# Kernel tuning notes

Hardware: AMD Instinct MI355X
Metric: run time of the kernel (lower is better)

## Reference

```python
import jax, jax.numpy as jnp
import numpy as np

H = 16       # num_heads
D = 128      # head_dim
SCALE = 1.0 / np.sqrt(D).astype(np.float32)


def setup_inputs() -> dict:
    key = jax.random.key(0)
    ks = jax.random.split(key, 5)
    B, S, C = 2, 2048, 2048
    x = jax.random.normal(ks[0], (B, S, C), dtype=jnp.float32)
    # nn.Linear stores weight as [out_features, in_features]; scale ~ kaiming-ish
    s = 1.0 / np.sqrt(C)
    wq = jax.random.normal(ks[1], (C, C), dtype=jnp.float32) * s
    wk = jax.random.normal(ks[2], (C, C), dtype=jnp.float32) * s
    wv = jax.random.normal(ks[3], (C, C), dtype=jnp.float32) * s
    wo = jax.random.normal(ks[4], (C, C), dtype=jnp.float32) * s
    return {"x": x, "wq": wq, "wk": wk, "wv": wv, "wo": wo}


def reference(x, wq, wk, wv, wo):
    B, S, C = x.shape
    # projections: nn.Linear(x) = x @ W.T
    q = (x @ wq.T).reshape(B, S, H, D).transpose(0, 2, 1, 3)  # [B,H,S,D]
    k = (x @ wk.T).reshape(B, S, H, D).transpose(0, 2, 1, 3)
    v = (x @ wv.T).reshape(B, S, H, D).transpose(0, 2, 1, 3)
    scores = jnp.einsum('bhqd,bhkd->bhqk', q, k) * SCALE      # [B,H,S,S]
    attn = jax.nn.softmax(scores, axis=-1)
    out = jnp.einsum('bhqk,bhkd->bhqd', attn, v)              # [B,H,S,D]
    out = out.transpose(0, 2, 1, 3).reshape(B, S, H * D)
    return out @ wo.T
```

## Files before the change

kernel.cpp:

```cpp
#include <hip/hip_runtime.h>
#include <hip/hip_bf16.h>
#include <cstdint>
#include <cstddef>

typedef __bf16 bf16_t;
typedef __bf16 bf8_t __attribute__((ext_vector_type(8)));
typedef float f4_t __attribute__((ext_vector_type(4)));
typedef float f8_t __attribute__((ext_vector_type(8)));

#define DEV static __device__ __forceinline__

DEV f4_t mfma16(bf8_t a, bf8_t b, f4_t c) {
    return __builtin_amdgcn_mfma_f32_16x16x32_bf16(a, b, c, 0, 0, 0);
}

DEV bf8_t cvt8(f8_t v) {
    bf8_t r;
#pragma unroll
    for (int i = 0; i < 8; ++i) r[i] = (bf16_t)v[i];
    return r;
}

DEV void load_lds16(const bf16_t* g, bf16_t* l) {
    __builtin_amdgcn_global_load_lds(
        (const __attribute__((address_space(1))) uint32_t*)g,
        (__attribute__((address_space(3))) uint32_t*)l,
        16, 0, 0);
}

__global__ __launch_bounds__(256) void cvt_fused(const float* __restrict__ x,
                                                 const float* __restrict__ wq,
                                                 const float* __restrict__ wk,
                                                 const float* __restrict__ wv,
                                                 bf16_t* __restrict__ xb,
                                                 bf16_t* __restrict__ wqkvb) {
    const int bid = blockIdx.x;
    const float* src;
    bf16_t* dst;
    int base;
    if (bid < 4096) {
        src = x; dst = xb; base = bid;
    } else {
        const int seg = (bid - 4096) >> 11;
        src = (seg == 0) ? wq : (seg == 1) ? wk : wv;
        dst = wqkvb + (size_t)seg * 4194304;
        base = (bid - 4096) & 2047;
    }
    const size_t i = ((size_t)base * 256 + threadIdx.x) * 8;
    const f8_t v = *(const f8_t*)&src[i];
    *(bf8_t*)&dst[i] = cvt8(v);
}

__global__ __launch_bounds__(256) void cvt_bf16(const float* __restrict__ in,
                                                bf16_t* __restrict__ out, int n8) {
    const int i = blockIdx.x * 256 + threadIdx.x;
    if (i < n8) {
        const f8_t v = *(const f8_t*)&in[(size_t)i * 8];
        *(bf8_t*)&out[(size_t)i * 8] = cvt8(v);
    }
}

DEV void stage_half(const bf16_t* X, int row0, int rb, int kt, bf16_t* bufX,
                    int wave, int srow, int scol) {
#pragma unroll
    for (int kk = 0; kk < 2; ++kk)
        load_lds16(X + (size_t)(row0 + rb + wave * 16 + srow) * 2048 + kt * 64 + kk * 32 + scol,
                   bufX + kk * 8192 + (rb + wave * 16) * 32);
}

__global__ __launch_bounds__(512, 2) void gemm256(const bf16_t* __restrict__ A,
                                                  const bf16_t* __restrict__ B,
                                                  bf16_t* __restrict__ Cq,
                                                  bf16_t* __restrict__ Ck,
                                                  bf16_t* __restrict__ Cv) {
    __shared__ bf16_t smem[65536];

    const int tid = threadIdx.x, lane = tid & 63, wave = tid >> 6;
    const int wr = wave >> 2, wc = wave & 3;
    const int q4 = lane >> 4, r16 = lane & 15;
    const int srow = lane >> 2;
    const int scol = ((lane & 3) ^ ((lane >> 3) & 3)) * 8;
    const int rkey = (r16 >> 1) & 3;

    int wg = blockIdx.y * 24 + blockIdx.x;
    wg = (wg & 7) * 48 + (wg >> 3);
    const int bm0 = (wg / 24) * 256;
    const int bn0 = (wg % 24) * 256;

    f4_t acc[8][4] = {};

    {
        bf16_t* b0 = smem;
        bf16_t* b1 = smem + 32768;
        stage_half(A, bm0, 0,   0, b0,          wave, srow, scol);
        stage_half(A, bm0, 128, 0, b0,          wave, srow, scol);
        stage_half(B, bn0, 0,   0, b0 + 16384,  wave, srow, scol);
        stage_half(B, bn0, 128, 0, b0 + 16384,  wave, srow, scol);
        stage_half(B, bn0, 0,   1, b1 + 16384,  wave, srow, scol);
        stage_half(B, bn0, 128, 1, b1 + 16384,  wave, srow, scol);
        asm volatile("s_waitcnt vmcnt(4)" ::: "memory");
        __builtin_amdgcn_s_barrier();
    }

    for (int t = 0; t < 32; ++t) {
        bf16_t* buf  = smem + (t & 1) * 32768;
        bf16_t* bufN = smem + ((t + 1) & 1) * 32768;

        bf8_t bq[4][2];
#pragma unroll
        for (int p = 0; p < 4; ++p) {
            if (p == 0) {
#pragma unroll
                for (int n = 0; n < 4; ++n)
#pragma unroll
                    for (int kk = 0; kk < 2; ++kk)
                        bq[n][kk] = *(const bf8_t*)&buf[16384 + kk * 8192 +
                                                       (wc * 64 + n * 16 + r16) * 32 +
                                                       (q4 ^ rkey) * 8];
            }
            bf8_t af[2][2];
#pragma unroll
            for (int i = 0; i < 2; ++i)
#pragma unroll
                for (int kk = 0; kk < 2; ++kk)
                    af[i][kk] = *(const bf8_t*)&buf[kk * 8192 +
                                                    (wr * 128 + (2 * p + i) * 16 + r16) * 32 +
                                                    (q4 ^ rkey) * 8];

            if (p == 0 && t + 1 < 32) {
                stage_half(A, bm0, 0,   t + 1, bufN, wave, srow, scol);
                stage_half(A, bm0, 128, t + 1, bufN, wave, srow, scol);
            }
            if (p == 1 && t + 2 < 32)
                stage_half(B, bn0, 0,   t + 2, buf + 16384, wave, srow, scol);
            if (p == 2 && t + 2 < 32)
                stage_half(B, bn0, 128, t + 2, buf + 16384, wave, srow, scol);

            __builtin_amdgcn_s_barrier();
            asm volatile("s_waitcnt lgkmcnt(0)" ::: "memory");
            __builtin_amdgcn_s_setprio(1);
#pragma unroll
            for (int kk = 0; kk < 2; ++kk)
#pragma unroll
                for (int i = 0; i < 2; ++i)
#pragma unroll
                    for (int n = 0; n < 4; ++n)
                        acc[2 * p + i][n] = mfma16(af[i][kk], bq[n][kk], acc[2 * p + i][n]);
            __builtin_amdgcn_s_setprio(0);
            if (p == 3) {
                if (t < 30) {
                    asm volatile("s_waitcnt vmcnt(4)" ::: "memory");
                } else {
                    asm volatile("s_waitcnt vmcnt(0)" ::: "memory");
                }
            }
            __builtin_amdgcn_s_barrier();
        }
    }

    __syncthreads();

    bf16_t* strip = smem + wave * 4608;
    if (bn0 < 4096) {
        bf16_t* dst = (bn0 < 2048) ? Cq : Ck;
        const int nb = (bn0 & 2047) + wc * 64;
#pragma unroll
        for (int P = 0; P < 2; ++P) {
#pragma unroll
            for (int i = 0; i < 4; ++i)
#pragma unroll
                for (int n = 0; n < 4; ++n)
#pragma unroll
                    for (int r = 0; r < 4; ++r)
                        strip[(i * 16 + q4 * 4 + r) * 72 + n * 16 + r16] =
                            (bf16_t)acc[P * 4 + i][n][r];
            asm volatile("s_waitcnt lgkmcnt(0)" ::: "memory");
#pragma unroll
            for (int it = 0; it < 8; ++it) {
                const int row = it * 8 + (lane >> 3);
                const int c = (lane & 7) * 8;
                *(bf8_t*)&dst[(size_t)(bm0 + wr * 128 + P * 64 + row) * 2048 + nb + c] =
                    *(const bf8_t*)&strip[row * 72 + c];
            }
            asm volatile("s_waitcnt lgkmcnt(0)" ::: "memory");
        }
    } else {
        const int bb = bm0 >> 11;
        const int s0 = bm0 & 2047;
#pragma unroll
        for (int P = 0; P < 2; ++P) {
#pragma unroll
            for (int i = 0; i < 4; ++i)
#pragma unroll
                for (int n = 0; n < 4; ++n)
#pragma unroll
                    for (int r = 0; r < 4; ++r)
                        strip[(n * 16 + r16) * 72 + i * 16 + q4 * 4 + r] =
                            (bf16_t)acc[P * 4 + i][n][r];
            asm volatile("s_waitcnt lgkmcnt(0)" ::: "memory");
#pragma unroll
            for (int it = 0; it < 8; ++it) {
                const int nrow = it * 8 + (lane >> 3);
                const int c = (lane & 7) * 8;
                const int dg = (bn0 - 4096) + wc * 64 + nrow;
                const int h = dg >> 7, d = dg & 127;
                *(bf8_t*)&Cv[(((size_t)(bb * 16 + h) * 128 + d) << 11) + s0 + wr * 128 + P * 64 + c] =
                    *(const bf8_t*)&strip[nrow * 72 + c];
            }
            asm volatile("s_waitcnt lgkmcnt(0)" ::: "memory");
        }
    }
}

template <int MODE>
__global__ __launch_bounds__(256) void gemm_m97(const bf16_t* __restrict__ A,
                                                const bf16_t* __restrict__ B,
                                                void* __restrict__ C0,
                                                bf16_t* __restrict__ C1,
                                                bf16_t* __restrict__ C2,
                                                int N, int K) {
    constexpr int SMEMN = (MODE == 0) ? 128 * 136 : 8192;
    __shared__ bf16_t smem[SMEMN];
    bf16_t* As = smem;
    bf16_t* Bs = smem + 4096;

    const int tid = threadIdx.x;
    const int lane = tid & 63;
    const int wave = tid >> 6;
    const int bm0 = blockIdx.y * 128;
    const int bn0 = blockIdx.x * 128;
    const int wm = (wave >> 1) * 64;
    const int wn = (wave & 1) * 64;
    const int q4 = lane >> 4;
    const int r16 = lane & 15;

    const int srow = lane >> 2;
    const int scol = (((lane & 3) ^ ((lane >> 3) & 3))) * 8;
    const int rkey = (r16 >> 1) & 3;

    f4_t acc[4][4] = {};

    for (int k0 = 0; k0 < K; k0 += 32) {
        __syncthreads();
        load_lds16(A + (size_t)(bm0 + wave * 16 + srow) * K + k0 + scol, As + wave * 16 * 32);
        load_lds16(A + (size_t)(bm0 + 64 + wave * 16 + srow) * K + k0 + scol,
                   As + (64 + wave * 16) * 32);
        load_lds16(B + (size_t)(bn0 + wave * 16 + srow) * K + k0 + scol, Bs + wave * 16 * 32);
        load_lds16(B + (size_t)(bn0 + 64 + wave * 16 + srow) * K + k0 + scol,
                   Bs + (64 + wave * 16) * 32);
        __syncthreads();

        bf8_t af[4], bfr[4];
#pragma unroll
        for (int i = 0; i < 4; ++i)
            af[i] = *(const bf8_t*)&As[(wm + i * 16 + r16) * 32 + (q4 ^ rkey) * 8];
#pragma unroll
        for (int j = 0; j < 4; ++j)
            bfr[j] = *(const bf8_t*)&Bs[(wn + j * 16 + r16) * 32 + (q4 ^ rkey) * 8];
#pragma unroll
        for (int i = 0; i < 4; ++i)
#pragma unroll
            for (int j = 0; j < 4; ++j)
                acc[i][j] = mfma16(af[i], bfr[j], acc[i][j]);
    }

    if (MODE == 1) {
        float* C = (float*)C0;
#pragma unroll
        for (int i = 0; i < 4; ++i)
#pragma unroll
            for (int j = 0; j < 4; ++j)
#pragma unroll
                for (int r = 0; r < 4; ++r) {
                    const int m = bm0 + wm + i * 16 + q4 * 4 + r;
                    const int n = bn0 + wn + j * 16 + r16;
                    C[(size_t)m * 2048 + n] = acc[i][j][r];
                }
        return;
    }

    __syncthreads();
    if (bn0 < 4096) {
        bf16_t* dst = (bn0 < 2048) ? (bf16_t*)C0 : C1;
        const int nbase = bn0 & 2047;
#pragma unroll
        for (int i = 0; i < 4; ++i)
#pragma unroll
            for (int j = 0; j < 4; ++j)
#pragma unroll
                for (int r = 0; r < 4; ++r)
                    smem[(wm + i * 16 + q4 * 4 + r) * 136 + wn + j * 16 + r16] =
                        (bf16_t)acc[i][j][r];
        __syncthreads();
#pragma unroll
        for (int it = 0; it < 8; ++it) {
            const int idx = it * 256 + tid;
            const int m = idx >> 4;
            const int nc = (idx & 15) * 8;
            *(bf8_t*)&dst[(size_t)(bm0 + m) * 2048 + nbase + nc] =
                *(const bf8_t*)&smem[m * 136 + nc];
        }
    } else {
#pragma unroll
        for (int i = 0; i < 4; ++i)
#pragma unroll
            for (int j = 0; j < 4; ++j)
#pragma unroll
                for (int r = 0; r < 4; ++r)
                    smem[(wn + j * 16 + r16) * 136 + wm + i * 16 + q4 * 4 + r] =
                        (bf16_t)acc[i][j][r];
        __syncthreads();
        const int bb = bm0 >> 11;
        const int s0 = bm0 & 2047;
        const int nh0 = bn0 - 4096;
#pragma unroll
        for (int it = 0; it < 8; ++it) {
            const int idx = it * 256 + tid;
            const int n = idx >> 4;
            const int mc = (idx & 15) * 8;
            const bf8_t v = *(const bf8_t*)&smem[n * 136 + mc];
            const int dg = nh0 + n;
            const int h = dg >> 7, d = dg & 127;
            *(bf8_t*)&C2[(((size_t)(bb * 16 + h) * 128 + d) << 11) + s0 + mc] = v;
        }
    }
}

__global__ __launch_bounds__(256) void flash5(const bf16_t* __restrict__ Q,
                                              const bf16_t* __restrict__ K,
                                              const bf16_t* __restrict__ VT,
                                              bf16_t* __restrict__ O) {
    constexpr int S = 2048, C = 2048;
    constexpr float SCL = 0.08838834764831845f * 1.4426950408889634f;
    __shared__ bf16_t Ks[4 * 64 * 32];
    __shared__ bf16_t Vs[2 * 128 * 32];
    __shared__ bf16_t Ps[4][32 * 72];

    const int tid = threadIdx.x, lane = tid & 63, wave = tid >> 6;
    const int q4 = lane >> 4, r16 = lane & 15;
    const int bh = blockIdx.y, b = bh >> 4, h = bh & 15;
    const int q0 = blockIdx.x * 128 + wave * 32;

    const size_t qrow = (size_t)b * S + q0;
    const bf16_t* Qp0 = Q + (qrow + r16) * C + h * 128;
    const bf16_t* Qp1 = Q + (qrow + 16 + r16) * C + h * 128;
    const bf16_t* Kbase = K + (size_t)b * S * C + h * 128;
    const bf16_t* Vbase = VT + (size_t)bh * 128 * S;
    bf16_t* Pw = &Ps[wave][0];

    const int srow = lane >> 2;
    const int scol = (((lane & 3) ^ ((lane >> 3) & 3))) * 8;
    const int rkey = (r16 >> 1) & 3;

    bf8_t aq0[4], aq1[4];
#pragma unroll
    for (int kk = 0; kk < 4; ++kk) {
        aq0[kk] = *(const bf8_t*)&Qp0[kk * 32 + q4 * 8];
        aq1[kk] = *(const bf8_t*)&Qp1[kk * 32 + q4 * 8];
    }

    bf8_t ones;
#pragma unroll
    for (int i = 0; i < 8; ++i) ones[i] = (bf16_t)1.0f;

    f4_t o0[8] = {}, o1[8] = {};
    f4_t lacc0 = {}, lacc1 = {};

    for (int kv0 = 0; kv0 < S; kv0 += 64) {
        __syncthreads();
#pragma unroll
        for (int r0 = 0; r0 < 64; r0 += 16)
            load_lds16(Kbase + (size_t)(kv0 + r0 + srow) * C + wave * 32 + scol,
                       Ks + wave * 2048 + r0 * 32);
        {
            const int kkp = wave >> 1;
            const int rb = (wave & 1) * 64;
#pragma unroll
            for (int r0 = 0; r0 < 64; r0 += 16)
                load_lds16(Vbase + (size_t)(rb + r0 + srow) * S + kv0 + kkp * 32 + scol,
                           Vs + kkp * 4096 + (rb + r0) * 32);
        }
        __syncthreads();

        f4_t s4a[4] = {}, s4b[4] = {};
#pragma unroll
        for (int kk = 0; kk < 4; ++kk) {
#pragma unroll
            for (int j = 0; j < 4; ++j) {
                const bf8_t bk =
                    *(const bf8_t*)&Ks[kk * 2048 + (j * 16 + r16) * 32 + (q4 ^ rkey) * 8];
                s4a[j] = mfma16(aq0[kk], bk, s4a[j]);
                s4b[j] = mfma16(aq1[kk], bk, s4b[j]);
            }
        }

#pragma unroll
        for (int r = 0; r < 4; ++r)
#pragma unroll
            for (int j = 0; j < 4; ++j) {
                Pw[(q4 * 4 + r) * 72 + j * 16 + r16] = (bf16_t)exp2f(s4a[j][r] * SCL);
                Pw[(16 + q4 * 4 + r) * 72 + j * 16 + r16] = (bf16_t)exp2f(s4b[j][r] * SCL);
            }
        asm volatile("s_waitcnt lgkmcnt(0)" ::: "memory");

        bf8_t ap0[2], ap1[2];
#pragma unroll
        for (int kkp = 0; kkp < 2; ++kkp) {
            ap0[kkp] = *(const bf8_t*)&Pw[r16 * 72 + kkp * 32 + q4 * 8];
            ap1[kkp] = *(const bf8_t*)&Pw[(16 + r16) * 72 + kkp * 32 + q4 * 8];
        }

#pragma unroll
        for (int kkp = 0; kkp < 2; ++kkp) {
            lacc0 = mfma16(ap0[kkp], ones, lacc0);
            lacc1 = mfma16(ap1[kkp], ones, lacc1);
        }

#pragma unroll
        for (int t = 0; t < 8; ++t) {
#pragma unroll
            for (int kkp = 0; kkp < 2; ++kkp) {
                const bf8_t bv =
                    *(const bf8_t*)&Vs[kkp * 4096 + (t * 16 + r16) * 32 + (q4 ^ rkey) * 8];
                o0[t] = mfma16(ap0[kkp], bv, o0[t]);
                o1[t] = mfma16(ap1[kkp], bv, o1[t]);
            }
        }
    }

    f4_t inv0, inv1;
#pragma unroll
    for (int r = 0; r < 4; ++r) {
        inv0[r] = 1.0f / lacc0[r];
        inv1[r] = 1.0f / lacc1[r];
    }
#pragma unroll
    for (int t = 0; t < 8; ++t)
#pragma unroll
        for (int r = 0; r < 4; ++r) {
            O[(qrow + q4 * 4 + r) * C + h * 128 + t * 16 + r16] = (bf16_t)(o0[t][r] * inv0[r]);
            O[(qrow + 16 + q4 * 4 + r) * C + h * 128 + t * 16 + r16] =
                (bf16_t)(o1[t][r] * inv1[r]);
        }
}

extern "C" void kernel_launch(void* const* d_in, const int* in_sizes, int n_in,
                              void* d_out, int out_size, void* d_ws, size_t ws_size,
                              hipStream_t stream) {
    const float* x  = (const float*)d_in[0];
    const float* wq = (const float*)d_in[1];
    const float* wk = (const float*)d_in[2];
    const float* wv = (const float*)d_in[3];
    const float* wo = (const float*)d_in[4];

    bf16_t* ws = (bf16_t*)d_ws;
    bf16_t* xb   = ws;
    bf16_t* Wqkv = ws + 8388608;
    bf16_t* Qb   = ws + 20971520;
    bf16_t* Kb   = ws + 29360128;
    bf16_t* Vt   = ws + 37748736;
    bf16_t* Wob  = xb;
    bf16_t* At   = Wqkv;

    cvt_fused<<<10240, 256, 0, stream>>>(x, wq, wk, wv, xb, Wqkv);

    gemm256<<<dim3(24, 16), 512, 0, stream>>>(xb, Wqkv, Qb, Kb, Vt);

    cvt_bf16<<<2048, 256, 0, stream>>>(wo, Wob, 524288);

    flash5<<<dim3(16, 32), 256, 0, stream>>>(Qb, Kb, Vt, At);

    gemm_m97<1><<<dim3(16, 32), 256, 0, stream>>>(At, Wob, d_out, nullptr, nullptr, 2048, 2048);
}
```

Before: 412.5 us.

## Shrink QKV GEMM tile to 128x256 to double workgroup count

```diff
diff --git a/kernel.cpp b/kernel.cpp
--- a/kernel.cpp
+++ b/kernel.cpp
@@ -60,20 +60,12 @@
     }
 }
 
-DEV void stage_half(const bf16_t* X, int row0, int rb, int kt, bf16_t* bufX,
-                    int wave, int srow, int scol) {
-#pragma unroll
-    for (int kk = 0; kk < 2; ++kk)
-        load_lds16(X + (size_t)(row0 + rb + wave * 16 + srow) * 2048 + kt * 64 + kk * 32 + scol,
-                   bufX + kk * 8192 + (rb + wave * 16) * 32);
-}
-
-__global__ __launch_bounds__(512, 2) void gemm256(const bf16_t* __restrict__ A,
-                                                  const bf16_t* __restrict__ B,
-                                                  bf16_t* __restrict__ Cq,
-                                                  bf16_t* __restrict__ Ck,
-                                                  bf16_t* __restrict__ Cv) {
-    __shared__ bf16_t smem[65536];
+__global__ __launch_bounds__(512, 2) void gemm_qkv(const bf16_t* __restrict__ A,
+                                                   const bf16_t* __restrict__ B,
+                                                   bf16_t* __restrict__ Cq,
+                                                   bf16_t* __restrict__ Ck,
+                                                   bf16_t* __restrict__ Cv) {
+    __shared__ bf16_t smem[49152];
 
     const int tid = threadIdx.x, lane = tid & 63, wave = tid >> 6;
     const int wr = wave >> 2, wc = wave & 3;
@@ -83,59 +75,60 @@
     const int rkey = (r16 >> 1) & 3;
 
     int wg = blockIdx.y * 24 + blockIdx.x;
-    wg = (wg & 7) * 48 + (wg >> 3);
-    const int bm0 = (wg / 24) * 256;
+    wg = (wg & 7) * 96 + (wg >> 3);
+    const int bm0 = (wg / 24) * 128;
     const int bn0 = (wg % 24) * 256;
 
-    f4_t acc[8][4] = {};
+    f4_t acc[4][4] = {};
+
+    auto stageA = [&](int kt, bf16_t* buf) {
+#pragma unroll
+        for (int kk = 0; kk < 2; ++kk)
+            load_lds16(A + (size_t)(bm0 + wave * 16 + srow) * 2048 + kt * 64 + kk * 32 + scol,
+                       buf + kk * 4096 + wave * 16 * 32);
+    };
+    auto stageB = [&](int kt, bf16_t* buf, int rb) {
+#pragma unroll
+        for (int kk = 0; kk < 2; ++kk)
+            load_lds16(B + (size_t)(bn0 + rb + wave * 16 + srow) * 2048 + kt * 64 + kk * 32 + scol,
+                       buf + 8192 + kk * 8192 + (rb + wave * 16) * 32);
+    };
 
     {
         bf16_t* b0 = smem;
-        bf16_t* b1 = smem + 32768;
-        stage_half(A, bm0, 0,   0, b0,          wave, srow, scol);
-        stage_half(A, bm0, 128, 0, b0,          wave, srow, scol);
-        stage_half(B, bn0, 0,   0, b0 + 16384,  wave, srow, scol);
-        stage_half(B, bn0, 128, 0, b0 + 16384,  wave, srow, scol);
-        stage_half(B, bn0, 0,   1, b1 + 16384,  wave, srow, scol);
-        stage_half(B, bn0, 128, 1, b1 + 16384,  wave, srow, scol);
+        bf16_t* b1 = smem + 24576;
+        stageA(0, b0);
+        stageB(0, b0, 0);
+        stageB(0, b0, 128);
+        stageB(1, b1, 0);
+        stageB(1, b1, 128);
         asm volatile("s_waitcnt vmcnt(4)" ::: "memory");
         __builtin_amdgcn_s_barrier();
     }
 
     for (int t = 0; t < 32; ++t) {
-        bf16_t* buf  = smem + (t & 1) * 32768;
-        bf16_t* bufN = smem + ((t + 1) & 1) * 32768;
+        bf16_t* buf  = smem + (t & 1) * 24576;
+        bf16_t* bufN = smem + ((t + 1) & 1) * 24576;
 
         bf8_t bq[4][2];
 #pragma unroll
-        for (int p = 0; p < 4; ++p) {
-            if (p == 0) {
-#pragma unroll
-                for (int n = 0; n < 4; ++n)
-#pragma unroll
-                    for (int kk = 0; kk < 2; ++kk)
-                        bq[n][kk] = *(const bf8_t*)&buf[16384 + kk * 8192 +
-                                                       (wc * 64 + n * 16 + r16) * 32 +
-                                                       (q4 ^ rkey) * 8];
-            }
+        for (int n = 0; n < 4; ++n)
+#pragma unroll
+            for (int kk = 0; kk < 2; ++kk)
+                bq[n][kk] = *(const bf8_t*)&buf[8192 + kk * 8192 +
+                                                (wc * 64 + n * 16 + r16) * 32 +
+                                                (q4 ^ rkey) * 8];
+
+        {
             bf8_t af[2][2];
 #pragma unroll
             for (int i = 0; i < 2; ++i)
 #pragma unroll
                 for (int kk = 0; kk < 2; ++kk)
-                    af[i][kk] = *(const bf8_t*)&buf[kk * 8192 +
-                                                    (wr * 128 + (2 * p + i) * 16 + r16) * 32 +
+                    af[i][kk] = *(const bf8_t*)&buf[kk * 4096 +
+                                                    (wr * 64 + i * 16 + r16) * 32 +
                                                     (q4 ^ rkey) * 8];
-
-            if (p == 0 && t + 1 < 32) {
-                stage_half(A, bm0, 0,   t + 1, bufN, wave, srow, scol);
-                stage_half(A, bm0, 128, t + 1, bufN, wave, srow, scol);
-            }
-            if (p == 1 && t + 2 < 32)
-                stage_half(B, bn0, 0,   t + 2, buf + 16384, wave, srow, scol);
-            if (p == 2 && t + 2 < 32)
-                stage_half(B, bn0, 128, t + 2, buf + 16384, wave, srow, scol);
-
+            if (t + 1 < 32) stageA(t + 1, bufN);
             __builtin_amdgcn_s_barrier();
             asm volatile("s_waitcnt lgkmcnt(0)" ::: "memory");
             __builtin_amdgcn_s_setprio(1);
@@ -145,14 +138,39 @@
                 for (int i = 0; i < 2; ++i)
 #pragma unroll
                     for (int n = 0; n < 4; ++n)
-                        acc[2 * p + i][n] = mfma16(af[i][kk], bq[n][kk], acc[2 * p + i][n]);
+                        acc[i][n] = mfma16(af[i][kk], bq[n][kk], acc[i][n]);
             __builtin_amdgcn_s_setprio(0);
-            if (p == 3) {
-                if (t < 30) {
-                    asm volatile("s_waitcnt vmcnt(4)" ::: "memory");
-                } else {
-                    asm volatile("s_waitcnt vmcnt(0)" ::: "memory");
-                }
+            __builtin_amdgcn_s_barrier();
+        }
+
+        {
+            bf8_t af[2][2];
+#pragma unroll
+            for (int i = 0; i < 2; ++i)
+#pragma unroll
+                for (int kk = 0; kk < 2; ++kk)
+                    af[i][kk] = *(const bf8_t*)&buf[kk * 4096 +
+                                                    (wr * 64 + (2 + i) * 16 + r16) * 32 +
+                                                    (q4 ^ rkey) * 8];
+            if (t + 2 < 32) {
+                stageB(t + 2, buf, 0);
+                stageB(t + 2, buf, 128);
+            }
+            __builtin_amdgcn_s_barrier();
+            asm volatile("s_waitcnt lgkmcnt(0)" ::: "memory");
+            __builtin_amdgcn_s_setprio(1);
+#pragma unroll
+            for (int kk = 0; kk < 2; ++kk)
+#pragma unroll
+                for (int i = 0; i < 2; ++i)
+#pragma unroll
+                    for (int n = 0; n < 4; ++n)
+                        acc[2 + i][n] = mfma16(af[i][kk], bq[n][kk], acc[2 + i][n]);
+            __builtin_amdgcn_s_setprio(0);
+            if (t < 30) {
+                asm volatile("s_waitcnt vmcnt(4)" ::: "memory");
+            } else {
+                asm volatile("s_waitcnt vmcnt(0)" ::: "memory");
             }
             __builtin_amdgcn_s_barrier();
         }
@@ -165,49 +183,41 @@
         bf16_t* dst = (bn0 < 2048) ? Cq : Ck;
         const int nb = (bn0 & 2047) + wc * 64;
 #pragma unroll
-        for (int P = 0; P < 2; ++P) {
-#pragma unroll
-            for (int i = 0; i < 4; ++i)
-#pragma unroll
-                for (int n = 0; n < 4; ++n)
-#pragma unroll
-                    for (int r = 0; r < 4; ++r)
-                        strip[(i * 16 + q4 * 4 + r) * 72 + n * 16 + r16] =
-                            (bf16_t)acc[P * 4 + i][n][r];
-            asm volatile("s_waitcnt lgkmcnt(0)" ::: "memory");
-#pragma unroll
-            for (int it = 0; it < 8; ++it) {
-                const int row = it * 8 + (lane >> 3);
-                const int c = (lane & 7) * 8;
-                *(bf8_t*)&dst[(size_t)(bm0 + wr * 128 + P * 64 + row) * 2048 + nb + c] =
-                    *(const bf8_t*)&strip[row * 72 + c];
-            }
-            asm volatile("s_waitcnt lgkmcnt(0)" ::: "memory");
+        for (int i = 0; i < 4; ++i)
+#pragma unroll
+            for (int n = 0; n < 4; ++n)
+#pragma unroll
+                for (int r = 0; r < 4; ++r)
+                    strip[(i * 16 + q4 * 4 + r) * 72 + n * 16 + r16] =
+                        (bf16_t)acc[i][n][r];
+        asm volatile("s_waitcnt lgkmcnt(0)" ::: "memory");
+#pragma unroll
+        for (int it = 0; it < 8; ++it) {
+            const int row = it * 8 + (lane >> 3);
+            const int c = (lane & 7) * 8;
+            *(bf8_t*)&dst[(size_t)(bm0 + wr * 64 + row) * 2048 + nb + c] =
+                *(const bf8_t*)&strip[row * 72 + c];
         }
     } else {
         const int bb = bm0 >> 11;
-        const int s0 = bm0 & 2047;
-#pragma unroll
-        for (int P = 0; P < 2; ++P) {
-#pragma unroll
-            for (int i = 0; i < 4; ++i)
-#pragma unroll
-                for (int n = 0; n < 4; ++n)
-#pragma unroll
-                    for (int r = 0; r < 4; ++r)
-                        strip[(n * 16 + r16) * 72 + i * 16 + q4 * 4 + r] =
-                            (bf16_t)acc[P * 4 + i][n][r];
-            asm volatile("s_waitcnt lgkmcnt(0)" ::: "memory");
-#pragma unroll
-            for (int it = 0; it < 8; ++it) {
-                const int nrow = it * 8 + (lane >> 3);
-                const int c = (lane & 7) * 8;
-                const int dg = (bn0 - 4096) + wc * 64 + nrow;
-                const int h = dg >> 7, d = dg & 127;
-                *(bf8_t*)&Cv[(((size_t)(bb * 16 + h) * 128 + d) << 11) + s0 + wr * 128 + P * 64 + c] =
-                    *(const bf8_t*)&strip[nrow * 72 + c];
-            }
-            asm volatile("s_waitcnt lgkmcnt(0)" ::: "memory");
+        const int s0 = (bm0 & 2047) + wr * 64;
+#pragma unroll
+        for (int i = 0; i < 4; ++i)
+#pragma unroll
+            for (int n = 0; n < 4; ++n)
+#pragma unroll
+                for (int r = 0; r < 4; ++r)
+                    strip[(n * 16 + r16) * 72 + i * 16 + q4 * 4 + r] =
+                        (bf16_t)acc[i][n][r];
+        asm volatile("s_waitcnt lgkmcnt(0)" ::: "memory");
+#pragma unroll
+        for (int it = 0; it < 8; ++it) {
+            const int nrow = it * 8 + (lane >> 3);
+            const int c = (lane & 7) * 8;
+            const int dg = (bn0 - 4096) + wc * 64 + nrow;
+            const int h = dg >> 7, d = dg & 127;
+            *(bf8_t*)&Cv[(((size_t)(bb * 16 + h) * 128 + d) << 11) + s0 + c] =
+                *(const bf8_t*)&strip[nrow * 72 + c];
         }
     }
 }
@@ -464,7 +474,7 @@
 
     cvt_fused<<<10240, 256, 0, stream>>>(x, wq, wk, wv, xb, Wqkv);
 
-    gemm256<<<dim3(24, 16), 512, 0, stream>>>(xb, Wqkv, Qb, Kb, Vt);
+    gemm_qkv<<<dim3(24, 32), 512, 0, stream>>>(xb, Wqkv, Qb, Kb, Vt);
 
     cvt_bf16<<<2048, 256, 0, stream>>>(wo, Wob, 524288);
 
```

Result: no change. 409.8 us (-0.7%).
